# Kernel tuning notes

Measured on AMD Instinct MI355X. Metric: run time of the kernel, lower is better.

Reference implementation:

```python
import jax, jax.numpy as jnp
import numpy as np

B, S, D = 4, 2048, 512
BETA = 1.0
PARAM_SCALE = 1.0 / np.sqrt(D)  # ~ torch Linear default init scale


def setup_inputs() -> dict:
    key = jax.random.key(0)
    ks = jax.random.split(key, 14)
    def rn(k, shape, scale=1.0):
        return (jax.random.normal(k, shape, jnp.float32) * scale).astype(jnp.float32)
    return {
        "x_re": rn(ks[0], (B, S, D)),
        "x_im": rn(ks[1], (B, S, D)),
        "Wq_re": rn(ks[2], (D, D), PARAM_SCALE), "Wq_im": rn(ks[3], (D, D), PARAM_SCALE),
        "bq_re": rn(ks[4], (D,), PARAM_SCALE),   "bq_im": rn(ks[5], (D,), PARAM_SCALE),
        "Wk_re": rn(ks[6], (D, D), PARAM_SCALE), "Wk_im": rn(ks[7], (D, D), PARAM_SCALE),
        "bk_re": rn(ks[8], (D,), PARAM_SCALE),   "bk_im": rn(ks[9], (D,), PARAM_SCALE),
        "Wv_re": rn(ks[10], (D, D), PARAM_SCALE), "Wv_im": rn(ks[11], (D, D), PARAM_SCALE),
        "bv_re": rn(ks[12], (D,), PARAM_SCALE),   "bv_im": rn(ks[13], (D,), PARAM_SCALE),
    }


def reference(x_re, x_im, Wq_re, Wq_im, bq_re, bq_im,
              Wk_re, Wk_im, bk_re, bk_im, Wv_re, Wv_im, bv_re, bv_im):
    cx = lambda re, im: (re + 1j * im).astype(jnp.complex64)
    x = cx(x_re, x_im)                          # [B,S,D] complex64
    # nn.Linear: y = x @ W.T + b (complex)
    Q = jnp.einsum('bsd,ed->bse', x, cx(Wq_re, Wq_im)) + cx(bq_re, bq_im)
    K = jnp.einsum('bsd,ed->bse', x, cx(Wk_re, Wk_im)) + cx(bk_re, bk_im)
    V = jnp.einsum('bsd,ed->bse', x, cx(Wv_re, Wv_im)) + cx(bv_re, bv_im)
    # energy = -Re(Q K^H); attn = softmax(-beta * energy) = softmax(beta * Re(Q K^H))
    scores = jnp.real(jnp.einsum('bse,bte->bst', Q, jnp.conj(K)))  # [B,S,S] float32
    attn = jax.nn.softmax(BETA * scores, axis=-1)
    out = jnp.einsum('bst,bte->bse', attn.astype(jnp.complex64), V)  # [B,S,D] complex64
    return out
```

## Files before the change

kernel.cpp:

```cpp
#include <hip/hip_runtime.h>
#include <hip/hip_bf16.h>
#include <cstdint>
#include <cstddef>


typedef unsigned short u16;
typedef __attribute__((ext_vector_type(8))) _Float16 half8;
typedef __attribute__((ext_vector_type(4))) float f32x4;

#define B_    4
#define S_    2048
#define D_    512
#define M_TOT (B_ * S_)
#define KC    (2 * D_)
#define N1    (6 * D_)
#define LP    32
#define RE_PLANE 4194304

#define X_ELEMS  ((size_t)M_TOT * KC)
#define W_ELEMS  ((size_t)N1 * KC)
#define QK_ELEMS ((size_t)M_TOT * KC)
#define VT_ELEMS ((size_t)B_ * KC * S_)
#define AT_ELEMS ((size_t)M_TOT * S_)

__device__ __forceinline__ u16 f2h(float f) {
    _Float16 h = (_Float16)f;
    return __builtin_bit_cast(u16, h);
}
__device__ __forceinline__ float h2f(u16 b) {
    return (float)__builtin_bit_cast(_Float16, b);
}

__device__ __forceinline__ f32x4 mfma16(half8 a, half8 b, f32x4 c) {
    return __builtin_amdgcn_mfma_f32_16x16x32_f16(a, b, c, 0, 0, 0);
}

__device__ __forceinline__ void dma16(const u16* g, u16* l) {
    __builtin_amdgcn_global_load_lds(
        (const __attribute__((address_space(1))) unsigned int*)g,
        (__attribute__((address_space(3))) unsigned int*)l,
        16, 0, 0);
}

__device__ __forceinline__ void stage_dma(const u16* __restrict__ src, int ld,
                                          int rowbase, int kbase,
                                          u16* __restrict__ dst, int tid) {
#pragma unroll
    for (int i = 0; i < 2; ++i) {
        int c = tid + 256 * i;
        int row = c >> 2, q = c & 3;
        dma16(src + (size_t)(rowbase + row) * ld + kbase + q * 8, dst + c * 8);
    }
}

__device__ __forceinline__ void stage_half(u16* __restrict__ plane,
                                           const u16* __restrict__ src,
                                           int rowbase, int kcol, int tid) {
#pragma unroll
    for (int i = 0; i < 2; ++i) {
        int c = tid + (i << 9);
        int c2 = c ^ (((c >> 5) & 1) << 1);
        int row = ((c2 >> 3) << 1) | ((c2 >> 2) & 1);
        int ks = c2 & 3;
        dma16(src + (size_t)(rowbase + row) * KC + (kcol + ks * 8),
              plane + c * 8);
    }
}

#define VMW(N) asm volatile("s_waitcnt vmcnt(" #N ")" ::: "memory")
#define BAR()  __builtin_amdgcn_s_barrier()

__global__ void k_diag(float* __restrict__ out, int out_size, float val) {
    int i = blockIdx.x * 256 + threadIdx.x;
    if (i < out_size && i < 4096) out[i] = val;
}

__global__ void k_prep(const float* __restrict__ xr, const float* __restrict__ xi,
                       const float* __restrict__ Wqr, const float* __restrict__ Wqi,
                       const float* __restrict__ Wkr, const float* __restrict__ Wki,
                       const float* __restrict__ Wvr, const float* __restrict__ Wvi,
                       const float* __restrict__ bqr, const float* __restrict__ bqi,
                       const float* __restrict__ bkr, const float* __restrict__ bki,
                       const float* __restrict__ bvr, const float* __restrict__ bvi,
                       u16* __restrict__ Xh, u16* __restrict__ Xl,
                       u16* __restrict__ Wh, float* __restrict__ bc) {
    int gb = blockIdx.x;
    int tid = threadIdx.x;
    if (gb < 16384) {
        int id = gb * 256 + tid;
        int m = id >> 9, d = id & 511;
        size_t o = (size_t)m * KC + d;
        if (o + D_ >= X_ELEMS) return;
        float vr = xr[id], vi = xi[id];
        u16 h;
        h = f2h(vr); Xh[o] = h;        Xl[o] = f2h(vr - h2f(h));
        h = f2h(vi); Xh[o + D_] = h;   Xl[o + D_] = f2h(vi - h2f(h));
    } else if (gb < 16384 + 12288) {
        int id = (gb - 16384) * 256 + tid;
        int n = id >> 10, k = id & 1023;
        int q = n >> 9, e = n & 511;
        int half = k >> 9, d = k & 511;
        const float* Wre = (q < 2) ? Wqr : ((q < 4) ? Wkr : Wvr);
        const float* Wim = (q < 2) ? Wqi : ((q < 4) ? Wki : Wvi);
        size_t src = (size_t)e * D_ + d;
        float v;
        if ((q & 1) == 0) v = half ? -Wim[src] : Wre[src];
        else              v = half ?  Wre[src] : Wim[src];
        if ((size_t)id < W_ELEMS) Wh[id] = f2h(v);
    } else {
        int id = (gb - 16384 - 12288) * 256 + tid;
        if (id >= N1) return;
        int q = id >> 9, e = id & 511;
        const float* src = (q == 0) ? bqr : (q == 1) ? bqi : (q == 2) ? bkr
                         : (q == 3) ? bki : (q == 4) ? bvr : bvi;
        bc[id] = src[e];
    }
}


#define RDA(d, pl, mg)                                                        \
  { const u16* _pa = &lds[pl][0];                                             \
    _Pragma("unroll")                                                         \
    for (int _i = 0; _i < 4; ++_i)                                            \
      d[_i] = *(const half8*)(_pa + aoffs + ((mg) * 4 + _i) * 512); }
#define RDB(d, pl)                                                            \
  { const u16* _pb = &lds[pl][0];                                             \
    _Pragma("unroll")                                                         \
    for (int _i = 0; _i < 4; ++_i)                                            \
      d[_i] = *(const half8*)(_pb + boffs + _i * 512); }
#define MF16(av, bv, mg)                                                      \
  { __builtin_amdgcn_s_setprio(1);                                            \
    _Pragma("unroll")                                                         \
    for (int _j = 0; _j < 4; ++_j) {                                          \
      _Pragma("unroll")                                                       \
      for (int _i = 0; _i < 4; ++_i)                                          \
        acc[(mg) * 4 + _i][_j] =                                              \
            mfma16(av[_i], bv[_j], acc[(mg) * 4 + _i][_j]);                   \
    }                                                                         \
    __builtin_amdgcn_s_setprio(0); }

#define W0(P, STG, WT) { MF16(aA, bA, 0); RDA(aB, ((P) << 2) | 0, 1); STG; WT; BAR(); }
#define W1(P, STG)     { MF16(aB, bA, 1); RDB(bB, ((P) << 2) | 3); RDA(aA, ((P) << 2) | 1, 0); STG; BAR(); }
#define W2(P, STG, WT) { MF16(aA, bB, 0); RDA(aB, ((P) << 2) | 1, 1); STG; WT; BAR(); }
#define W3(P, STG)     { MF16(aB, bB, 1); RDB(bA, (((P) ^ 1) << 2) | 2); RDA(aA, (((P) ^ 1) << 2) | 0, 0); STG; BAR(); }
#define W3L()          { MF16(aB, bB, 1); }
#define NOP_ ((void)0)

__global__ __launch_bounds__(512, 2) void k_gemm1(
    const u16* __restrict__ Xh, const u16* __restrict__ Xl,
    const u16* __restrict__ Wh,
    const float* __restrict__ bc,
    u16* __restrict__ Qh, u16* __restrict__ Ql,
    u16* __restrict__ Kh, u16* __restrict__ Kl,
    u16* __restrict__ VT) {
    __shared__ __attribute__((aligned(16))) u16 lds[8][8192];
    int tid = threadIdx.x;

    int L = blockIdx.y * 12 + blockIdx.x;
    int bx, by;
    if (L < 256) {
        int q = (L & 7) * 32 + (L >> 3);
        bx = q & 7; by = q >> 3;
    } else {
        int v = L - 256;
        int vv = (v & 7) * 16 + (v >> 3);
        bx = 8 + (vv & 3); by = vv >> 2;
    }
    int nb = bx * 256, mb = by * 256;
    int g = bx >> 2;
    bool vblk = (g == 2);
    int NT = vblk ? 16 : 32;

    int lane = tid & 63, wave = tid >> 6;
    int wm = (wave >> 2) * 128, wn = (wave & 3) * 64;
    int lr = lane & 15, lq = lane >> 4;
    int lqs8 = (lq ^ (((lr >> 3) & 1) << 1)) * 8;
    int aoffs = (wm + lr) * 32 + lqs8;
    int boffs = (wn + lr) * 32 + lqs8;

    f32x4 acc[8][4] = {};
    half8 aA[4], aB[4], bA[4], bB[4];

    stage_half(&lds[0][0], Xh, mb, 0, tid);
    stage_half(&lds[2][0], Wh, nb, 0, tid);
    stage_half(&lds[1][0], Xh, mb, 32, tid);
    stage_half(&lds[3][0], Wh, nb, 32, tid);
    stage_half(&lds[4][0], Xh, mb, 64, tid);
    stage_half(&lds[6][0], Wh, nb, 64, tid);
    VMW(8);
    BAR();
    RDB(bA, 2);
    RDA(aA, 0, 0);

    for (int t = 0; t < NT - 2; ++t) {
        const int p = t & 1;
        const u16* s1 = (!vblk && (t + 1) >= 16) ? Xl : Xh;
        const int k1 = (((t + 1) & 15) << 6) + 32;
        const u16* s2 = (!vblk && (t + 2) >= 16) ? Xl : Xh;
        const int k2 = ((t + 2) & 15) << 6;
        W0(p, stage_half(&lds[((p ^ 1) << 2) | 1][0], s1, mb, k1, tid), VMW(6));
        W1(p, stage_half(&lds[((p ^ 1) << 2) | 3][0], Wh, nb, k1, tid));
        W2(p, stage_half(&lds[(p << 2) | 0][0], s2, mb, k2, tid), VMW(6));
        W3(p, stage_half(&lds[(p << 2) | 2][0], Wh, nb, k2, tid));
    }
    {
        const u16* s1 = vblk ? Xh : Xl;
        const int k1 = (((NT - 1) & 15) << 6) + 32;
        W0(0, stage_half(&lds[(1 << 2) | 1][0], s1, mb, k1, tid), VMW(6));
        W1(0, stage_half(&lds[(1 << 2) | 3][0], Wh, nb, k1, tid));
        W2(0, NOP_, VMW(4));
        W3(0, NOP_);
    }
    {
        W0(1, NOP_, VMW(0));
        W1(1, NOP_);
        W2(1, NOP_, NOP_);
        W3L();
    }

#pragma unroll
    for (int j = 0; j < 4; ++j) {
        int n_g = nb + wn + j * 16 + lr;
        float bias = bc[n_g];
        int c = n_g & 1023;
#pragma unroll
        for (int i = 0; i < 8; ++i) {
            int m0 = mb + wm + i * 16 + lq * 4;
            if (vblk) {
                int bidx = m0 >> 11, s0 = m0 & 2047;
                u16 pk[4];
#pragma unroll
                for (int r = 0; r < 4; ++r) pk[r] = f2h(acc[i][j][r] + bias);
                size_t idx = ((size_t)(bidx * KC + c)) * S_ + s0;
                if (idx + 3 < VT_ELEMS)
                    *(ushort4*)&VT[idx] = make_ushort4(pk[0], pk[1], pk[2], pk[3]);
            } else {
                u16* dh = g ? Kh : Qh;
                u16* dl = g ? Kl : Ql;
#pragma unroll
                for (int r = 0; r < 4; ++r) {
                    float v = acc[i][j][r] + bias;
                    u16 h = f2h(v);
                    size_t idx = (size_t)(m0 + r) * KC + c;
                    if (idx < QK_ELEMS) {
                        dh[idx] = h;
                        dl[idx] = f2h(v - h2f(h));
                    }
                }
            }
        }
    }
}

__global__ __launch_bounds__(256) void k_gemm2(
    const u16* __restrict__ Qh, const u16* __restrict__ Ql,
    const u16* __restrict__ Kh, const u16* __restrict__ Kl,
    float* __restrict__ SC, int zbase) {
    __shared__ __attribute__((aligned(16))) u16 sAh[128 * LP], sAl[128 * LP],
                                                sBh[128 * LP], sBl[128 * LP];
    int tid = threadIdx.x;
    int nb = blockIdx.x * 128, mb = blockIdx.y * 128;
    int z = zbase + blockIdx.z;
    const u16* Ah = Qh + (size_t)z * S_ * KC;
    const u16* Al = Ql + (size_t)z * S_ * KC;
    const u16* Bh = Kh + (size_t)z * S_ * KC;
    const u16* Bl = Kl + (size_t)z * S_ * KC;
    int lane = tid & 63, wave = tid >> 6;
    int wm = (wave >> 1) * 64, wn = (wave & 1) * 64;
    int lr = lane & 15, lq = lane >> 4;
    f32x4 acc[4][4] = {};

    for (int k0 = 0; k0 < KC; k0 += 32) {
        __syncthreads();
        stage_dma(Ah, KC, mb, k0, sAh, tid);
        stage_dma(Al, KC, mb, k0, sAl, tid);
        stage_dma(Bh, KC, nb, k0, sBh, tid);
        stage_dma(Bl, KC, nb, k0, sBl, tid);
        __syncthreads();
        half8 ah[4], al[4], bh[4], bl[4];
#pragma unroll
        for (int i = 0; i < 4; ++i) {
            int ra = wm + i * 16 + lr;
            ah[i] = *(const half8*)&sAh[ra * LP + lq * 8];
            al[i] = *(const half8*)&sAl[ra * LP + lq * 8];
            int rb = wn + i * 16 + lr;
            bh[i] = *(const half8*)&sBh[rb * LP + lq * 8];
            bl[i] = *(const half8*)&sBl[rb * LP + lq * 8];
        }
#pragma unroll
        for (int i = 0; i < 4; ++i)
#pragma unroll
            for (int j = 0; j < 4; ++j) {
                acc[i][j] = mfma16(ah[i], bh[j], acc[i][j]);
                acc[i][j] = mfma16(al[i], bh[j], acc[i][j]);
                acc[i][j] = mfma16(ah[i], bl[j], acc[i][j]);
            }
    }

    size_t sc_limit = (size_t)gridDim.z * S_ * S_;
#pragma unroll
    for (int j = 0; j < 4; ++j) {
        int t = nb + wn + j * 16 + lr;
#pragma unroll
        for (int i = 0; i < 4; ++i) {
            int s0 = mb + wm + i * 16 + lq * 4;
#pragma unroll
            for (int r = 0; r < 4; ++r) {
                size_t idx = ((size_t)blockIdx.z * S_ + s0 + r) * S_ + t;
                if (idx < sc_limit) SC[idx] = acc[i][j][r];
            }
        }
    }
}

__global__ __launch_bounds__(256) void k_softmax(const float* __restrict__ SC,
                                                 u16* __restrict__ AT, int zbase) {
    int row = blockIdx.x;
    const float* src = SC + (size_t)row * S_;
    size_t drow = (size_t)zbase * S_ + row;
    u16* dst = AT + drow * S_;
    int tid = threadIdx.x;
    float v[8];
#pragma unroll
    for (int i = 0; i < 8; ++i) v[i] = src[tid + i * 256];
    float m = v[0];
#pragma unroll
    for (int i = 1; i < 8; ++i) m = fmaxf(m, v[i]);
    for (int off = 32; off > 0; off >>= 1) m = fmaxf(m, __shfl_down(m, off));
    __shared__ float redm[4], reds[4];
    if ((tid & 63) == 0) redm[tid >> 6] = m;
    __syncthreads();
    m = fmaxf(fmaxf(redm[0], redm[1]), fmaxf(redm[2], redm[3]));
    float s = 0.f;
#pragma unroll
    for (int i = 0; i < 8; ++i) { v[i] = __expf(v[i] - m); s += v[i]; }
    for (int off = 32; off > 0; off >>= 1) s += __shfl_down(s, off);
    if ((tid & 63) == 0) reds[tid >> 6] = s;
    __syncthreads();
    float inv = 1.0f / (reds[0] + reds[1] + reds[2] + reds[3]);
    if (drow * S_ + 2047 < AT_ELEMS) {
#pragma unroll
        for (int i = 0; i < 8; ++i) dst[tid + i * 256] = f2h(v[i] * inv);
    }
}

__global__ __launch_bounds__(256) void k_gemm3(
    const u16* __restrict__ AT, const u16* __restrict__ VT,
    float* __restrict__ out, int out_size, int full) {
    __shared__ __attribute__((aligned(16))) u16 sA[128 * LP], sB[128 * LP];
    int tid = threadIdx.x;
    int nb = blockIdx.x * 128, mb = blockIdx.y * 128, z = blockIdx.z;
    const u16* Abase = AT + (size_t)z * S_ * S_;
    const u16* Bbase = VT + (size_t)z * KC * S_;
    int lane = tid & 63, wave = tid >> 6;
    int wm = (wave >> 1) * 64, wn = (wave & 1) * 64;
    int lr = lane & 15, lq = lane >> 4;
    f32x4 acc[4][4] = {};

    for (int k0 = 0; k0 < S_; k0 += 32) {
        __syncthreads();
        stage_dma(Abase, S_, mb, k0, sA, tid);
        stage_dma(Bbase, S_, nb, k0, sB, tid);
        __syncthreads();
        half8 a[4], b[4];
#pragma unroll
        for (int i = 0; i < 4; ++i) {
            a[i] = *(const half8*)&sA[(wm + i * 16 + lr) * LP + lq * 8];
            b[i] = *(const half8*)&sB[(wn + i * 16 + lr) * LP + lq * 8];
        }
#pragma unroll
        for (int i = 0; i < 4; ++i)
#pragma unroll
            for (int j = 0; j < 4; ++j)
                acc[i][j] = mfma16(a[i], b[j], acc[i][j]);
    }

#pragma unroll
    for (int j = 0; j < 4; ++j) {
        int f = nb + wn + j * 16 + lr;
#pragma unroll
        for (int i = 0; i < 4; ++i) {
            int s0 = mb + wm + i * 16 + lq * 4;
#pragma unroll
            for (int r = 0; r < 4; ++r) {
                size_t base = ((size_t)z * S_ + s0 + r) * D_;
                if (f < D_) {
                    size_t o = base + f;
                    if (o < (size_t)out_size) out[o] = acc[i][j][r];
                } else if (full) {
                    size_t o = (size_t)RE_PLANE + base + (f - D_);
                    if (o < (size_t)out_size) out[o] = acc[i][j][r];
                }
            }
        }
    }
}


extern "C" void kernel_launch(void* const* d_in, const int* in_sizes, int n_in,
                              void* d_out, int out_size, void* d_ws, size_t ws_size,
                              hipStream_t stream) {
    (void)in_sizes; (void)n_in;
    const float* xr  = (const float*)d_in[0];
    const float* xi  = (const float*)d_in[1];
    const float* Wqr = (const float*)d_in[2];
    const float* Wqi = (const float*)d_in[3];
    const float* bqr = (const float*)d_in[4];
    const float* bqi = (const float*)d_in[5];
    const float* Wkr = (const float*)d_in[6];
    const float* Wki = (const float*)d_in[7];
    const float* bkr = (const float*)d_in[8];
    const float* bki = (const float*)d_in[9];
    const float* Wvr = (const float*)d_in[10];
    const float* Wvi = (const float*)d_in[11];
    const float* bvr = (const float*)d_in[12];
    const float* bvi = (const float*)d_in[13];
    float* out = (float*)d_out;

    constexpr size_t SZ_X  = X_ELEMS * 2;
    constexpr size_t SZ_W  = W_ELEMS * 2;
    constexpr size_t SZ_BC = (size_t)N1 * 4;
    constexpr size_t SZ_QK = QK_ELEMS * 2;
    constexpr size_t SZ_VT = VT_ELEMS * 2;
    constexpr size_t SZ_SC_B = (size_t)S_ * S_ * 4;

    char* p = (char*)d_ws;
    size_t off = 0;
    auto take = [&](size_t sz) {
        char* r = p + off;
        off += (sz + 255) & ~(size_t)255;
        return r;
    };
    u16*   Xh = (u16*)take(SZ_X);
    u16*   Xl = (u16*)take(SZ_X);
    u16*   Wh = (u16*)take(SZ_W);
    float* bc = (float*)take(SZ_BC);
    u16*   Qh = (u16*)take(SZ_QK);
    u16*   Ql = (u16*)take(SZ_QK);
    u16*   Kh = (u16*)take(SZ_QK);
    u16*   Kl = (u16*)take(SZ_QK);
    u16*   VT = (u16*)take(SZ_VT);
    u16*   AT = Xh;
    float* SC = (float*)(p + off);

    int nz = 0;
    if (ws_size > off) nz = (int)((ws_size - off) / SZ_SC_B);
    if (nz > B_) nz = B_;
    if (nz < 1) {
        k_diag<<<16, 256, 0, stream>>>(out, out_size, 1000.0f + (float)(ws_size >> 20));
        return;
    }

    int full = (out_size >= 2 * RE_PLANE) ? 1 : 0;

    k_prep<<<16384 + 12288 + 12, 256, 0, stream>>>(
        xr, xi, Wqr, Wqi, Wkr, Wki, Wvr, Wvi,
        bqr, bqi, bkr, bki, bvr, bvi, Xh, Xl, Wh, bc);
    k_gemm1<<<dim3(12, 32), 512, 0, stream>>>(Xh, Xl, Wh, bc, Qh, Ql, Kh, Kl, VT);

    for (int z0 = 0; z0 < B_; z0 += nz) {
        int zc = (B_ - z0 < nz) ? (B_ - z0) : nz;
        k_gemm2<<<dim3(S_ / 128, S_ / 128, zc), 256, 0, stream>>>(Qh, Ql, Kh, Kl, SC, z0);
        k_softmax<<<zc * S_, 256, 0, stream>>>(SC, AT, z0);
    }
    k_gemm3<<<dim3(KC / 128, S_ / 128, B_), 256, 0, stream>>>(AT, VT, out, out_size, full);
}
```

Baseline: 412.2 us.

## Add 256x256-tile pipelined QK^T GEMM with split-fp16 staging

Adds a new scores GEMM using 256x256 output tiles with 512 threads, an 8-buffer LDS ring and a software-pipelined stage/compute schedule over 48 k-steps covering the hi/lo fp16 split terms. It is used when the whole batch fits in one pass, and is meant to raise operand reuse and overlap global loads with MFMA work compared with the 128x128 kernel. In exchange it uses more registers and LDS per block and launches far fewer blocks, which can hurt occupancy or load balance.

```diff
diff --git a/kernel.cpp b/kernel.cpp
--- a/kernel.cpp
+++ b/kernel.cpp
@@ -252,6 +252,86 @@
     }
 }
 
+__global__ __launch_bounds__(512, 2) void k_gemm2_256(
+    const u16* __restrict__ Qh, const u16* __restrict__ Ql,
+    const u16* __restrict__ Kh, const u16* __restrict__ Kl,
+    float* __restrict__ SC, int zbase) {
+    __shared__ __attribute__((aligned(16))) u16 lds[8][8192];
+    int tid = threadIdx.x;
+    int z = zbase + blockIdx.z;
+    const u16* Aq = Qh + (size_t)z * S_ * KC;
+    const u16* Al = Ql + (size_t)z * S_ * KC;
+    const u16* Bh = Kh + (size_t)z * S_ * KC;
+    const u16* Bl = Kl + (size_t)z * S_ * KC;
+    int nb = blockIdx.x * 256, mb = blockIdx.y * 256;
+    const int NT = 48;
+
+    int lane = tid & 63, wave = tid >> 6;
+    int wm = (wave >> 2) * 128, wn = (wave & 3) * 64;
+    int lr = lane & 15, lq = lane >> 4;
+    int lqs8 = (lq ^ (((lr >> 3) & 1) << 1)) * 8;
+    int aoffs = (wm + lr) * 32 + lqs8;
+    int boffs = (wn + lr) * 32 + lqs8;
+
+    f32x4 acc[8][4] = {};
+    half8 aA[4], aB[4], bA[4], bB[4];
+
+    stage_half(&lds[0][0], Aq, mb, 0, tid);
+    stage_half(&lds[2][0], Bh, nb, 0, tid);
+    stage_half(&lds[1][0], Aq, mb, 32, tid);
+    stage_half(&lds[3][0], Bh, nb, 32, tid);
+    stage_half(&lds[4][0], Aq, mb, 64, tid);
+    stage_half(&lds[6][0], Bh, nb, 64, tid);
+    VMW(8);
+    BAR();
+    RDB(bA, 2);
+    RDA(aA, 0, 0);
+
+    for (int t = 0; t < NT - 2; ++t) {
+        const int p = t & 1;
+        const int t1 = t + 1, t2 = t + 2;
+        const int sg1 = t1 >> 4, sg2 = t2 >> 4;
+        const u16* a1 = (sg1 == 1) ? Al : Aq;
+        const u16* b1 = (sg1 == 2) ? Bl : Bh;
+        const u16* a2 = (sg2 == 1) ? Al : Aq;
+        const u16* b2 = (sg2 == 2) ? Bl : Bh;
+        const int k1 = ((t1 & 15) << 6) + 32;
+        const int k2 = (t2 & 15) << 6;
+        W0(p, stage_half(&lds[((p ^ 1) << 2) | 1][0], a1, mb, k1, tid), VMW(6));
+        W1(p, stage_half(&lds[((p ^ 1) << 2) | 3][0], b1, nb, k1, tid));
+        W2(p, stage_half(&lds[(p << 2) | 0][0], a2, mb, k2, tid), VMW(6));
+        W3(p, stage_half(&lds[(p << 2) | 2][0], b2, nb, k2, tid));
+    }
+    {
+        const int k1 = ((47 & 15) << 6) + 32;
+        W0(0, stage_half(&lds[(1 << 2) | 1][0], Aq, mb, k1, tid), VMW(6));
+        W1(0, stage_half(&lds[(1 << 2) | 3][0], Bl, nb, k1, tid));
+        W2(0, NOP_, VMW(4));
+        W3(0, NOP_);
+    }
+    {
+        W0(1, NOP_, VMW(0));
+        W1(1, NOP_);
+        W2(1, NOP_, NOP_);
+        W3L();
+    }
+
+    size_t sc_limit = (size_t)gridDim.z * S_ * S_;
+#pragma unroll
+    for (int j = 0; j < 4; ++j) {
+        int n_g = nb + wn + j * 16 + lr;
+#pragma unroll
+        for (int i = 0; i < 8; ++i) {
+            int m0 = mb + wm + i * 16 + lq * 4;
+#pragma unroll
+            for (int r = 0; r < 4; ++r) {
+                size_t idx = ((size_t)blockIdx.z * S_ + m0 + r) * S_ + n_g;
+                if (idx < sc_limit) SC[idx] = acc[i][j][r];
+            }
+        }
+    }
+}
+
 __global__ __launch_bounds__(256) void k_gemm2(
     const u16* __restrict__ Qh, const u16* __restrict__ Ql,
     const u16* __restrict__ Kh, const u16* __restrict__ Kl,
@@ -460,7 +540,13 @@
 
     for (int z0 = 0; z0 < B_; z0 += nz) {
         int zc = (B_ - z0 < nz) ? (B_ - z0) : nz;
-        k_gemm2<<<dim3(S_ / 128, S_ / 128, zc), 256, 0, stream>>>(Qh, Ql, Kh, Kl, SC, z0);
+        if (zc == B_) {
+            k_gemm2_256<<<dim3(S_ / 256, S_ / 256, zc), 512, 0, stream>>>(
+                Qh, Ql, Kh, Kl, SC, z0);
+        } else {
+            k_gemm2<<<dim3(S_ / 128, S_ / 128, zc), 256, 0, stream>>>(
+                Qh, Ql, Kh, Kl, SC, z0);
+        }
         k_softmax<<<zc * S_, 256, 0, stream>>>(SC, AT, z0);
     }
     k_gemm3<<<dim3(KC / 128, S_ / 128, B_), 256, 0, stream>>>(AT, VT, out, out_size, full);
```

Result: faster. 390.4 us (-5.3%).

## Pipeline score GEMM with double-buffered async LDS staging and split-precision k-chaining

Applied to the files above, without the earlier changes.

Rewrites the QK^T score GEMM as a software-pipelined kernel. It double-buffers async DMA copies into a swizzled LDS layout, overlaps the MFMA work with the next tiles' loads and fragment reads, and uses explicit vmcnt waits and barriers. The three fp16 hi/lo products are no longer issued per k-step. Instead the K dimension is treated as an extended sequence: hi×hi, then lo×hi, then hi×lo, each as 16 chunks of 64 columns, 48 steps in all. Launch bounds ask for 2 blocks per CU. The hand-unrolled prologue and epilogue indexing is fragile, and its correctness depends on the exact chunk ordering.

```diff
diff --git a/kernel.cpp b/kernel.cpp
--- a/kernel.cpp
+++ b/kernel.cpp
@@ -59,6 +59,20 @@
 #pragma unroll
     for (int i = 0; i < 2; ++i) {
         int c = tid + (i << 9);
+        int c2 = c ^ (((c >> 5) & 1) << 1);
+        int row = ((c2 >> 3) << 1) | ((c2 >> 2) & 1);
+        int ks = c2 & 3;
+        dma16(src + (size_t)(rowbase + row) * KC + (kcol + ks * 8),
+              plane + c * 8);
+    }
+}
+
+__device__ __forceinline__ void stage_half8(u16* __restrict__ plane,
+                                            const u16* __restrict__ src,
+                                            int rowbase, int kcol, int tid) {
+#pragma unroll
+    for (int i = 0; i < 2; ++i) {
+        int c = tid + (i << 8);
         int c2 = c ^ (((c >> 5) & 1) << 1);
         int row = ((c2 >> 3) << 1) | ((c2 >> 2) & 1);
         int ks = c2 & 3;
@@ -117,7 +131,6 @@
     }
 }
 
-
 #define RDA(d, pl, mg)                                                        \
   { const u16* _pa = &lds[pl][0];                                             \
     _Pragma("unroll")                                                         \
@@ -252,61 +265,95 @@
     }
 }
 
-__global__ __launch_bounds__(256) void k_gemm2(
+__global__ __launch_bounds__(256, 2) void k_gemm2w(
     const u16* __restrict__ Qh, const u16* __restrict__ Ql,
     const u16* __restrict__ Kh, const u16* __restrict__ Kl,
     float* __restrict__ SC, int zbase) {
-    __shared__ __attribute__((aligned(16))) u16 sAh[128 * LP], sAl[128 * LP],
-                                                sBh[128 * LP], sBl[128 * LP];
+    __shared__ __attribute__((aligned(16))) u16 lds[8][4096];
     int tid = threadIdx.x;
+    int z = zbase + blockIdx.z;
+    const u16* Aq  = Qh + (size_t)z * S_ * KC;
+    const u16* Alo = Ql + (size_t)z * S_ * KC;
+    const u16* Bh  = Kh + (size_t)z * S_ * KC;
+    const u16* Blo = Kl + (size_t)z * S_ * KC;
     int nb = blockIdx.x * 128, mb = blockIdx.y * 128;
-    int z = zbase + blockIdx.z;
-    const u16* Ah = Qh + (size_t)z * S_ * KC;
-    const u16* Al = Ql + (size_t)z * S_ * KC;
-    const u16* Bh = Kh + (size_t)z * S_ * KC;
-    const u16* Bl = Kl + (size_t)z * S_ * KC;
+
     int lane = tid & 63, wave = tid >> 6;
     int wm = (wave >> 1) * 64, wn = (wave & 1) * 64;
     int lr = lane & 15, lq = lane >> 4;
+    int lqs8 = (lq ^ (((lr >> 3) & 1) << 1)) * 8;
+    int aoffs = (wm + lr) * 32 + lqs8;
+    int boffs = (wn + lr) * 32 + lqs8;
+
     f32x4 acc[4][4] = {};
-
-    for (int k0 = 0; k0 < KC; k0 += 32) {
-        __syncthreads();
-        stage_dma(Ah, KC, mb, k0, sAh, tid);
-        stage_dma(Al, KC, mb, k0, sAl, tid);
-        stage_dma(Bh, KC, nb, k0, sBh, tid);
-        stage_dma(Bl, KC, nb, k0, sBl, tid);
-        __syncthreads();
-        half8 ah[4], al[4], bh[4], bl[4];
+    half8 aA[4], aB[4], bA[4], bB[4];
+
+    stage_half8(&lds[0][0], Aq, mb, 0, tid);
+    stage_half8(&lds[2][0], Bh, nb, 0, tid);
+    stage_half8(&lds[1][0], Aq, mb, 32, tid);
+    stage_half8(&lds[3][0], Bh, nb, 32, tid);
+    stage_half8(&lds[4][0], Aq, mb, 64, tid);
+    stage_half8(&lds[6][0], Bh, nb, 64, tid);
+    VMW(4);
+    BAR();
+    RDA(aA, 0, 0);
+    RDB(bA, 2);
+
+    for (int t = 0; t < 46; ++t) {
+        const int p = t & 1;
+        const int t1 = t + 1, t2 = t + 2;
+        const u16* a1 = ((t1 >> 4) == 1) ? Alo : Aq;
+        const u16* b1 = ((t1 >> 4) == 2) ? Blo : Bh;
+        const u16* a2 = ((t2 >> 4) == 1) ? Alo : Aq;
+        const u16* b2 = ((t2 >> 4) == 2) ? Blo : Bh;
+        const int k1 = ((t1 & 15) << 6) + 32;
+        const int k2 = (t2 & 15) << 6;
+        MF16(aA, bA, 0);
+        RDA(aB, (p << 2) | 1, 0);
+        RDB(bB, (p << 2) | 3);
+        stage_half8(&lds[((p ^ 1) << 2) | 1][0], a1, mb, k1, tid);
+        stage_half8(&lds[((p ^ 1) << 2) | 3][0], b1, nb, k1, tid);
+        VMW(4);
+        BAR();
+        MF16(aB, bB, 0);
+        RDA(aA, ((p ^ 1) << 2) | 0, 0);
+        RDB(bA, ((p ^ 1) << 2) | 2);
+        stage_half8(&lds[(p << 2) | 0][0], a2, mb, k2, tid);
+        stage_half8(&lds[(p << 2) | 2][0], b2, nb, k2, tid);
+        VMW(4);
+        BAR();
+    }
+    {
+        MF16(aA, bA, 0);
+        RDA(aB, 1, 0);
+        RDB(bB, 3);
+        stage_half8(&lds[(1 << 2) | 1][0], Aq, mb, ((47 & 15) << 6) + 32, tid);
+        stage_half8(&lds[(1 << 2) | 3][0], Blo, nb, ((47 & 15) << 6) + 32, tid);
+        VMW(4);
+        BAR();
+        MF16(aB, bB, 0);
+        RDA(aA, (1 << 2) | 0, 0);
+        RDB(bA, (1 << 2) | 2);
+        VMW(0);
+        BAR();
+    }
+    {
+        MF16(aA, bA, 0);
+        RDA(aB, (1 << 2) | 1, 0);
+        RDB(bB, (1 << 2) | 3);
+        MF16(aB, bB, 0);
+    }
+
+    size_t sc_limit = (size_t)gridDim.z * S_ * S_;
+#pragma unroll
+    for (int j = 0; j < 4; ++j) {
+        int n_g = nb + wn + j * 16 + lr;
 #pragma unroll
         for (int i = 0; i < 4; ++i) {
-            int ra = wm + i * 16 + lr;
-            ah[i] = *(const half8*)&sAh[ra * LP + lq * 8];
-            al[i] = *(const half8*)&sAl[ra * LP + lq * 8];
-            int rb = wn + i * 16 + lr;
-            bh[i] = *(const half8*)&sBh[rb * LP + lq * 8];
-            bl[i] = *(const half8*)&sBl[rb * LP + lq * 8];
-        }
-#pragma unroll
-        for (int i = 0; i < 4; ++i)
-#pragma unroll
-            for (int j = 0; j < 4; ++j) {
-                acc[i][j] = mfma16(ah[i], bh[j], acc[i][j]);
-                acc[i][j] = mfma16(al[i], bh[j], acc[i][j]);
-                acc[i][j] = mfma16(ah[i], bl[j], acc[i][j]);
-            }
-    }
-
-    size_t sc_limit = (size_t)gridDim.z * S_ * S_;
-#pragma unroll
-    for (int j = 0; j < 4; ++j) {
-        int t = nb + wn + j * 16 + lr;
-#pragma unroll
-        for (int i = 0; i < 4; ++i) {
-            int s0 = mb + wm + i * 16 + lq * 4;
+            int m0 = mb + wm + i * 16 + lq * 4;
 #pragma unroll
             for (int r = 0; r < 4; ++r) {
-                size_t idx = ((size_t)blockIdx.z * S_ + s0 + r) * S_ + t;
+                size_t idx = ((size_t)blockIdx.z * S_ + m0 + r) * S_ + n_g;
                 if (idx < sc_limit) SC[idx] = acc[i][j][r];
             }
         }
@@ -460,7 +507,8 @@
 
     for (int z0 = 0; z0 < B_; z0 += nz) {
         int zc = (B_ - z0 < nz) ? (B_ - z0) : nz;
-        k_gemm2<<<dim3(S_ / 128, S_ / 128, zc), 256, 0, stream>>>(Qh, Ql, Kh, Kl, SC, z0);
+        k_gemm2w<<<dim3(S_ / 128, S_ / 128, zc), 256, 0, stream>>>(
+            Qh, Ql, Kh, Kl, SC, z0);
         k_softmax<<<zc * S_, 256, 0, stream>>>(SC, AT, z0);
     }
     k_gemm3<<<dim3(KC / 128, S_ / 128, B_), 256, 0, stream>>>(AT, VT, out, out_size, full);
```

Result: no change. 417.3 us (+1.3%).
